# Performance work log

Hardware: AMD Instinct MI355X
Metric: run time of the kernel (lower is better)

Reference implementation:

```python
import jax, jax.numpy as jnp
import numpy as np

BN_EPS = 1e-5


def conv1x1(x, W, b):
    # x: (B, Cin, H, Wd); W: (Cout, Cin); b: (Cout,)
    return jnp.einsum('bchw,oc->bohw', x, W) + b[None, :, None, None]


def maxpool2x2(x):
    B, C, H, Wd = x.shape
    return x.reshape(B, C, H // 2, 2, Wd // 2, 2).max(axis=(3, 5))


def batchnorm_train(x, gamma, beta):
    # training-mode BN over (B, H, W) per channel, NCHW
    mean = x.mean(axis=(0, 2, 3), keepdims=True)
    var = x.var(axis=(0, 2, 3), keepdims=True)
    xn = (x - mean) * jax.lax.rsqrt(var + BN_EPS)
    return xn * gamma[None, :, None, None] + beta[None, :, None, None]


def setup_inputs() -> dict:
    key = jax.random.key(0)
    ks = jax.random.split(key, 11)
    C, Ci = 256, 128
    scale = 1.0 / np.sqrt(C)
    x = jax.random.normal(ks[0], (4, C, 96, 96), dtype=jnp.float32)
    Wg = jax.random.normal(ks[1], (Ci, C), dtype=jnp.float32) * scale
    bg = jax.random.normal(ks[2], (Ci,), dtype=jnp.float32) * 0.01
    Wt = jax.random.normal(ks[3], (Ci, C), dtype=jnp.float32) * scale
    bt = jax.random.normal(ks[4], (Ci,), dtype=jnp.float32) * 0.01
    Wp = jax.random.normal(ks[5], (Ci, C), dtype=jnp.float32) * scale
    bp = jax.random.normal(ks[6], (Ci,), dtype=jnp.float32) * 0.01
    Ww = jax.random.normal(ks[7], (C, Ci), dtype=jnp.float32) * (1.0 / np.sqrt(Ci))
    bw = jax.random.normal(ks[8], (C,), dtype=jnp.float32) * 0.01
    gamma = jax.random.uniform(ks[9], (C,), dtype=jnp.float32)
    beta = jax.random.normal(ks[10], (C,), dtype=jnp.float32) * 0.01
    return {'x': x, 'Wg': Wg, 'bg': bg, 'Wt': Wt, 'bt': bt, 'Wp': Wp,
            'bp': bp, 'Ww': Ww, 'bw': bw, 'gamma': gamma, 'beta': beta}


def reference(x, Wg, bg, Wt, bt, Wp, bp, Ww, bw, gamma, beta):
    B, C, H, Wd = x.shape
    Ci = Wg.shape[0]
    # g, phi: 1x1 conv then 2x2 maxpool (sub_sample_factor=2)
    g_x = maxpool2x2(conv1x1(x, Wg, bg)).reshape(B, Ci, -1)          # (B, Ci, M)
    phi_x = maxpool2x2(conv1x1(x, Wp, bp)).reshape(B, Ci, -1)        # (B, Ci, M)
    theta_x = conv1x1(x, Wt, bt).reshape(B, Ci, -1)                  # (B, Ci, N)
    # embedded-gaussian attention: softmax(theta^T phi) g^T
    f = jnp.einsum('bcn,bcm->bnm', theta_x, phi_x)                   # (B, N, M)
    a = jax.nn.softmax(f, axis=-1)
    y = jnp.einsum('bnm,bcm->bcn', a, g_x).reshape(B, Ci, H, Wd)
    # W: 1x1 conv + BN (training-mode batch stats), then residual
    W_y = batchnorm_train(conv1x1(y, Ww, bw), gamma, beta)
    return W_y + x
```

## Files before the change

kernel.cpp:

```cpp
#include <hip/hip_runtime.h>
#include <hip/hip_bf16.h>

#define BB 4
#define CC 256
#define CI 128
#define NPIX 9216
#define MPIX 2304
#define WIMG 96
#define WPOOL 48
#define LOG2E 1.4426950408889634f

typedef _Float16 f16x2 __attribute__((ext_vector_type(2)));
typedef _Float16 f16x4 __attribute__((ext_vector_type(4)));
typedef _Float16 f16x8 __attribute__((ext_vector_type(8)));
typedef float f32x4 __attribute__((ext_vector_type(4)));

static __device__ __forceinline__ void gload16(const void* g, void* lds) {
  __builtin_amdgcn_global_load_lds(
      (const __attribute__((address_space(1))) unsigned int*)g,
      (__attribute__((address_space(3))) unsigned int*)lds, 16, 0, 0);
}

__global__ __launch_bounds__(256) void k_prep(
    const float* __restrict__ Wt, const float* __restrict__ Wg,
    const float* __restrict__ Wp, const float* __restrict__ Ww,
    _Float16* __restrict__ Wall, _Float16* __restrict__ Wwh)
{
  int i = blockIdx.x * 256 + threadIdx.x;
  if (i < 98304) {
    int o = i >> 8, c = i & 255;
    float v = (o < 128) ? Wt[o * 256 + c]
            : (o < 256) ? Wg[(o - 128) * 256 + c]
                        : Wp[(o - 256) * 256 + c];
    Wall[i] = (_Float16)v;
  } else {
    int j = i - 98304;
    Wwh[j] = (_Float16)Ww[j];
  }
}

__global__ __launch_bounds__(256) void k_xt(
    const float* __restrict__ x, _Float16* __restrict__ xt)
{
  const int nt = blockIdx.x, ct = blockIdx.y, b = blockIdx.z;
  const int n0 = nt * 64, c0 = ct * 64;
  __shared__ float L[64][65];
  const int t = threadIdx.x;
  #pragma unroll
  for (int i = 0; i < 16; ++i) {
    int idx = i * 256 + t, c = idx >> 6, n = idx & 63;
    L[c][n] = x[(size_t)(b * CC + c0 + c) * NPIX + n0 + n];
  }
  __syncthreads();
  #pragma unroll
  for (int i = 0; i < 4; ++i) {
    int idx = i * 256 + t, n = idx >> 4, cg = idx & 15;
    f16x4 v;
    v[0] = (_Float16)L[cg * 4 + 0][n]; v[1] = (_Float16)L[cg * 4 + 1][n];
    v[2] = (_Float16)L[cg * 4 + 2][n]; v[3] = (_Float16)L[cg * 4 + 3][n];
    *(f16x4*)&xt[(size_t)(b * NPIX + n0 + n) * 256 + c0 + cg * 4] = v;
  }
}

__global__ __launch_bounds__(256) void k_convA(
    const _Float16* __restrict__ xt, const _Float16* __restrict__ Wall,
    const float* __restrict__ bt, const float* __restrict__ bg,
    const float* __restrict__ bp,
    _Float16* __restrict__ th_h, _Float16* __restrict__ gphi)
{
  const int pt = blockIdx.x, ot = blockIdx.y, b = blockIdx.z;
  const int p0 = pt * 128, o0 = ot * 128;
  __shared__ char smem[34816];
  char* WsB = smem;
  char* XsB = smem + 8192;
  const int tid = threadIdx.x;
  const int l = tid & 63, w = tid >> 6;
  const int l15 = l & 15, g16 = l >> 4;
  const int wo = (w & 1) * 64, wp = (w >> 1) * 64;

  f32x4 acc[4][4] = {};
  for (int k0 = 0; k0 < 256; k0 += 32) {
    #pragma unroll
    for (int i = 0; i < 2; ++i) {
      int idx = i * 256 + tid, r = idx >> 2, cg = idx & 3;
      int sw = (cg ^ ((r >> 1) & 3)) * 16;
      *(int4*)(WsB + r * 64 + sw) =
          *(const int4*)&Wall[(size_t)(o0 + r) * 256 + k0 + cg * 8];
      *(int4*)(XsB + r * 64 + sw) =
          *(const int4*)&xt[(size_t)(b * NPIX + p0 + r) * 256 + k0 + cg * 8];
    }
    __syncthreads();
    f16x8 af[4], bf[4];
    #pragma unroll
    for (int f = 0; f < 4; ++f) {
      int ro = wo + f * 16 + l15;
      af[f] = *(const f16x8*)(WsB + ro * 64 + ((g16 ^ ((ro >> 1) & 3)) * 16));
      int rp = wp + f * 16 + l15;
      bf[f] = *(const f16x8*)(XsB + rp * 64 + ((g16 ^ ((rp >> 1) & 3)) * 16));
    }
    #pragma unroll
    for (int of = 0; of < 4; ++of)
      #pragma unroll
      for (int pf = 0; pf < 4; ++pf)
        acc[of][pf] = __builtin_amdgcn_mfma_f32_16x16x32_f16(af[of], bf[pf], acc[of][pf], 0, 0, 0);
    __syncthreads();
  }

  if (o0 == 0) {
    _Float16* T = (_Float16*)smem;
    #pragma unroll
    for (int of = 0; of < 4; ++of) {
      const float4 bb = *(const float4*)&bt[wo + of * 16 + g16 * 4];
      float bv[4] = {bb.x, bb.y, bb.z, bb.w};
      #pragma unroll
      for (int pf = 0; pf < 4; ++pf) {
        f16x4 v;
        #pragma unroll
        for (int r = 0; r < 4; ++r)
          v[r] = (_Float16)((acc[of][pf][r] + bv[r]) * LOG2E);
        *(f16x4*)&T[(wp + pf * 16 + l15) * 136 + wo + of * 16 + g16 * 4] = v;
      }
    }
    __syncthreads();
    #pragma unroll
    for (int i = 0; i < 8; ++i) {
      int idx = i * 256 + tid, row = idx >> 4, cg = idx & 15;
      *(int4*)&th_h[(size_t)(b * NPIX + p0 + row) * 128 + cg * 8] =
          *(const int4*)&T[row * 136 + cg * 8];
    }
  } else {
    const float* bsel = (o0 == 128) ? bg : bp;
    const int chbase = o0 - 128;
    #pragma unroll
    for (int of = 0; of < 4; ++of) {
      const float4 bb = *(const float4*)&bsel[wo + of * 16 + g16 * 4];
      float bv[4] = {bb.x, bb.y, bb.z, bb.w};
      #pragma unroll
      for (int pf = 0; pf < 4; ++pf)
        #pragma unroll
        for (int r = 0; r < 4; ++r) {
          int ch = chbase + wo + of * 16 + g16 * 4 + r;
          gphi[(size_t)(b * 256 + ch) * NPIX + p0 + wp + pf * 16 + l15] =
              (_Float16)(acc[of][pf][r] + bv[r]);
        }
    }
  }
}

__global__ __launch_bounds__(256) void k_pool2(
    const _Float16* __restrict__ gphi,
    _Float16* __restrict__ g_h, _Float16* __restrict__ phi_h)
{
  const int mt = blockIdx.x, ct = blockIdx.y, b = blockIdx.z;
  const int m0 = mt * 64, c0 = ct * 32;
  __shared__ _Float16 Lg[32][72], Lp[32][72];
  const int t = threadIdx.x;
  #pragma unroll
  for (int i = 0; i < 8; ++i) {
    int idx = i * 256 + t, c = idx >> 6, m = idx & 63;
    int mm = m0 + m, hp = mm / WPOOL, wp = mm % WPOOL;
    const _Float16* sg = &gphi[(size_t)(b * 256 + c0 + c) * NPIX + hp * 192 + wp * 2];
    f16x2 a0 = *(const f16x2*)sg;
    f16x2 a1 = *(const f16x2*)(sg + WIMG);
    Lg[c][m] = (_Float16)fmaxf(fmaxf((float)a0[0], (float)a0[1]),
                               fmaxf((float)a1[0], (float)a1[1]));
    const _Float16* sp = sg + (size_t)128 * NPIX;
    f16x2 b0 = *(const f16x2*)sp;
    f16x2 b1 = *(const f16x2*)(sp + WIMG);
    Lp[c][m] = (_Float16)fmaxf(fmaxf((float)b0[0], (float)b0[1]),
                               fmaxf((float)b1[0], (float)b1[1]));
  }
  __syncthreads();
  {
    int c = t >> 3, mq = t & 7;
    f16x8 v = *(const f16x8*)&Lg[c][mq * 8];
    *(f16x8*)&g_h[(size_t)(b * CI + c0 + c) * MPIX + m0 + mq * 8] = v;
  }
  #pragma unroll
  for (int i = 0; i < 2; ++i) {
    int idx = i * 256 + t, m = idx >> 3, cg = idx & 7;
    f16x4 v;
    v[0] = Lp[cg * 4 + 0][m]; v[1] = Lp[cg * 4 + 1][m];
    v[2] = Lp[cg * 4 + 2][m]; v[3] = Lp[cg * 4 + 3][m];
    *(f16x4*)&phi_h[(size_t)(b * MPIX + m0 + m) * 128 + c0 + cg * 4] = v;
  }
}

__global__ __launch_bounds__(256, 2) void k_attn(
    const _Float16* __restrict__ th_h,
    const _Float16* __restrict__ phi_h,
    const _Float16* __restrict__ g_h,
    _Float16* __restrict__ y_part,
    float2* __restrict__ ml)
{
  const int qt = blockIdx.x, b = blockIdx.y, split = blockIdx.z;
  const int n0 = qt * 128;
  const int kt0 = split * 18;
  __shared__ char smem[49152];
  char* const GlB = smem + 16384;
  char* const PlB = smem + 32768;

  const int tid = threadIdx.x;
  const int l = tid & 63, wid = tid >> 6;
  const int l15 = l & 15, g16 = l >> 4;
  const int wq0 = wid * 32;

  f16x8 thf[2][4];
  #pragma unroll
  for (int qh = 0; qh < 2; ++qh) {
    const size_t row = (size_t)(b * NPIX + n0 + wq0 + 16 * qh + l15) * 128;
    #pragma unroll
    for (int cs = 0; cs < 4; ++cs)
      thf[qh][cs] = *(const f16x8*)&th_h[row + 32 * cs + 8 * g16];
  }

  auto stage_phi = [&](int kt) {
    const int m1 = kt * 64;
    #pragma unroll
    for (int j = 0; j < 4; ++j) {
      int mbase = wid * 16 + j * 4;
      int m = mbase + (l >> 4);
      int cg = (l & 15) ^ (m & 7);
      gload16(&phi_h[((size_t)(b * MPIX + m1 + m) << 7) + cg * 8],
              smem + mbase * 256);
    }
  };
  auto stage_g = [&](int kt) {
    const int m1 = kt * 64;
    #pragma unroll
    for (int j = 0; j < 4; ++j) {
      int cbase = wid * 32 + j * 8;
      int c = cbase + (l >> 3);
      int cg = (l & 7) ^ (c & 7);
      gload16(&g_h[(size_t)(b * CI + c) * MPIX + m1 + cg * 8],
              GlB + cbase * 128);
    }
  };

  stage_phi(kt0);
  __syncthreads();

  f32x4 yacc[2][8] = {};
  float mrun[2] = {-1e30f, -1e30f};
  float lrun[2] = {0.f, 0.f};

  #pragma unroll 1
  for (int kt = kt0; kt < kt0 + 18; ++kt) {
    stage_g(kt);

    f32x4 sacc[4][2] = {};
    #pragma unroll
    for (int cs = 0; cs < 4; ++cs) {
      const int cb = cs * 64 + g16 * 16;
      #pragma unroll
      for (int mf = 0; mf < 4; ++mf) {
        const int m = 16 * mf + l15;
        f16x8 aph = *(const f16x8*)(smem + m * 256 + (cb ^ ((m & 7) << 4)));
        sacc[mf][0] = __builtin_amdgcn_mfma_f32_16x16x32_f16(aph, thf[0][cs], sacc[mf][0], 0, 0, 0);
        sacc[mf][1] = __builtin_amdgcn_mfma_f32_16x16x32_f16(aph, thf[1][cs], sacc[mf][1], 0, 0, 0);
      }
    }

    float mx[2];
    #pragma unroll
    for (int qh = 0; qh < 2; ++qh) {
      float m0 = -1e30f;
      #pragma unroll
      for (int mf = 0; mf < 4; ++mf)
        #pragma unroll
        for (int r = 0; r < 4; ++r) m0 = fmaxf(m0, sacc[mf][qh][r]);
      m0 = fmaxf(m0, __shfl_xor(m0, 16, 64));
      m0 = fmaxf(m0, __shfl_xor(m0, 32, 64));
      mx[qh] = m0;
    }
    const int nskip = !__all((mx[0] <= mrun[0] + 8.f) & (mx[1] <= mrun[1] + 8.f));
    if (nskip) {
      float scl2[2];
      #pragma unroll
      for (int qh = 0; qh < 2; ++qh) {
        const float mn = fmaxf(mrun[qh], mx[qh]);
        scl2[qh] = exp2f(mrun[qh] - mn);
        lrun[qh] *= scl2[qh];
        mrun[qh] = mn;
      }
      float rs[2][4];
      #pragma unroll
      for (int r = 0; r < 4; ++r) {
        rs[0][r] = __shfl(scl2[0], 4 * g16 + r, 64);
        rs[1][r] = __shfl(scl2[1], 4 * g16 + r, 64);
      }
      #pragma unroll
      for (int qi = 0; qi < 2; ++qi)
        #pragma unroll
        for (int cf = 0; cf < 8; ++cf)
          #pragma unroll
          for (int r = 0; r < 4; ++r)
            yacc[qi][cf][r] *= rs[qi][r];
    }

    f16x4 pr[4][2];
    #pragma unroll
    for (int qh = 0; qh < 2; ++qh) {
      float sum = 0.f;
      #pragma unroll
      for (int mf = 0; mf < 4; ++mf)
        #pragma unroll
        for (int r = 0; r < 4; ++r) {
          float p = exp2f(sacc[mf][qh][r] - mrun[qh]);
          _Float16 ph = (_Float16)p;
          pr[mf][qh][r] = ph;
          sum += (float)ph;
        }
      sum += __shfl_xor(sum, 16, 64);
      sum += __shfl_xor(sum, 32, 64);
      lrun[qh] += sum;
    }

    #pragma unroll
    for (int qh = 0; qh < 2; ++qh) {
      const int qw = l15 + 16 * qh;
      char* prow = PlB + (wid << 12) + qw * 128;
      #pragma unroll
      for (int mf = 0; mf < 4; ++mf)
        *(f16x4*)(prow + ((32 * mf + 8 * g16) ^ ((qw & 7) << 4))) = pr[mf][qh];
    }

    __syncthreads();

    if (kt + 1 < kt0 + 18)
      stage_phi(kt + 1);

    #pragma unroll
    for (int ms = 0; ms < 2; ++ms) {
      const int mb = ms * 64 + g16 * 16;
      const int q0w = l15, q1w = l15 + 16;
      f16x8 pa0 = *(const f16x8*)(PlB + (wid << 12) + q0w * 128 + (mb ^ ((q0w & 7) << 4)));
      f16x8 pa1 = *(const f16x8*)(PlB + (wid << 12) + q1w * 128 + (mb ^ ((q1w & 7) << 4)));
      #pragma unroll
      for (int cf = 0; cf < 8; ++cf) {
        const int c = 16 * cf + l15;
        f16x8 gb = *(const f16x8*)(GlB + c * 128 + (mb ^ ((c & 7) << 4)));
        yacc[0][cf] = __builtin_amdgcn_mfma_f32_16x16x32_f16(pa0, gb, yacc[0][cf], 0, 0, 0);
        yacc[1][cf] = __builtin_amdgcn_mfma_f32_16x16x32_f16(pa1, gb, yacc[1][cf], 0, 0, 0);
      }
    }

    __syncthreads();
  }

  if (g16 == 0) {
    #pragma unroll
    for (int qh = 0; qh < 2; ++qh)
      ml[(size_t)(split * BB + b) * NPIX + n0 + wq0 + 16 * qh + l15] =
          make_float2(mrun[qh], lrun[qh]);
  }
  _Float16* Yl = (_Float16*)smem;
  #pragma unroll
  for (int qi = 0; qi < 2; ++qi)
    #pragma unroll
    for (int cf = 0; cf < 8; ++cf)
      #pragma unroll
      for (int r = 0; r < 4; ++r)
        Yl[(wq0 + 16 * qi + 4 * g16 + r) * 136 + 16 * cf + l15] =
            (_Float16)yacc[qi][cf][r];
  __syncthreads();
  #pragma unroll
  for (int i = 0; i < 8; ++i) {
    int idx = i * 256 + tid, row = idx >> 4, cg = idx & 15;
    *(int4*)&y_part[(size_t)((split * BB + b) * NPIX + n0 + row) * 128 + cg * 8] =
        *(const int4*)&Yl[row * 136 + cg * 8];
  }
}

__global__ __launch_bounds__(256) void k_comb(
    const _Float16* __restrict__ y_part, const float2* __restrict__ ml,
    _Float16* __restrict__ y_h)
{
  int idx = blockIdx.x * 256 + threadIdx.x;
  int cg = idx & 15;
  int n  = (idx >> 4) % NPIX;
  int b  = (idx >> 4) / NPIX;
  float2 a0 = ml[(size_t)b * NPIX + n];
  float2 a1 = ml[(size_t)(BB + b) * NPIX + n];
  float M = fmaxf(a0.x, a1.x);
  float w0 = exp2f(a0.x - M), w1 = exp2f(a1.x - M);
  float inv = 1.0f / (w0 * a0.y + w1 * a1.y);
  w0 *= inv; w1 *= inv;
  f16x8 v0 = *(const f16x8*)&y_part[(size_t)(b * NPIX + n) * 128 + cg * 8];
  f16x8 v1 = *(const f16x8*)&y_part[(size_t)((BB + b) * NPIX + n) * 128 + cg * 8];
  f16x8 o;
  #pragma unroll
  for (int r = 0; r < 8; ++r)
    o[r] = (_Float16)(w0 * (float)v0[r] + w1 * (float)v1[r]);
  *(f16x8*)&y_h[(size_t)(b * NPIX + n) * 128 + cg * 8] = o;
}

__global__ __launch_bounds__(256) void k_wconv(
    const _Float16* __restrict__ y_h, const _Float16* __restrict__ Wwh,
    const float* __restrict__ bw, float* __restrict__ zbuf)
{
  const int nt = blockIdx.x, ot = blockIdx.y, b = blockIdx.z;
  const int n0 = nt * 128, o0 = ot * 128;
  __shared__ char smem[16384];
  char* WsB = smem;
  char* YsB = smem + 8192;
  const int tid = threadIdx.x;
  const int l = tid & 63, w = tid >> 6;
  const int l15 = l & 15, g16 = l >> 4;
  const int wo = (w & 1) * 64, wn = (w >> 1) * 64;

  f32x4 acc[4][4] = {};
  for (int k0 = 0; k0 < 128; k0 += 32) {
    #pragma unroll
    for (int i = 0; i < 2; ++i) {
      int idx = i * 256 + tid, r = idx >> 2, cg = idx & 3;
      int sw = (cg ^ ((r >> 1) & 3)) * 16;
      *(int4*)(WsB + r * 64 + sw) =
          *(const int4*)&Wwh[(size_t)(o0 + r) * 128 + k0 + cg * 8];
      *(int4*)(YsB + r * 64 + sw) =
          *(const int4*)&y_h[(size_t)(b * NPIX + n0 + r) * 128 + k0 + cg * 8];
    }
    __syncthreads();
    f16x8 af[4], bf[4];
    #pragma unroll
    for (int f = 0; f < 4; ++f) {
      int ro = wo + f * 16 + l15;
      af[f] = *(const f16x8*)(WsB + ro * 64 + ((g16 ^ ((ro >> 1) & 3)) * 16));
      int rn = wn + f * 16 + l15;
      bf[f] = *(const f16x8*)(YsB + rn * 64 + ((g16 ^ ((rn >> 1) & 3)) * 16));
    }
    #pragma unroll
    for (int of = 0; of < 4; ++of)
      #pragma unroll
      for (int pf = 0; pf < 4; ++pf)
        acc[of][pf] = __builtin_amdgcn_mfma_f32_16x16x32_f16(af[of], bf[pf], acc[of][pf], 0, 0, 0);
    __syncthreads();
  }
  #pragma unroll
  for (int of = 0; of < 4; ++of) {
    const float4 bb = *(const float4*)&bw[o0 + wo + of * 16 + g16 * 4];
    float bv[4] = {bb.x, bb.y, bb.z, bb.w};
    #pragma unroll
    for (int pf = 0; pf < 4; ++pf)
      #pragma unroll
      for (int r = 0; r < 4; ++r)
        zbuf[(size_t)(b * CC + o0 + wo + of * 16 + g16 * 4 + r) * NPIX +
             n0 + wn + pf * 16 + l15] = acc[of][pf][r] + bv[r];
  }
}

__global__ __launch_bounds__(256) void k_stats(
    const float* __restrict__ zbuf, float* __restrict__ stats)
{
  const int o = blockIdx.x, t = threadIdx.x;
  float s = 0.f, s2 = 0.f;
  for (int b = 0; b < BB; ++b) {
    const float* z = &zbuf[(size_t)(b * CC + o) * NPIX];
    for (int i = t; i < NPIX / 4; i += 256) {
      float4 v = *(const float4*)&z[i * 4];
      s  += v.x + v.y + v.z + v.w;
      s2 += v.x * v.x + v.y * v.y + v.z * v.z + v.w * v.w;
    }
  }
  #pragma unroll
  for (int off = 1; off < 64; off <<= 1) {
    s  += __shfl_xor(s,  off, 64);
    s2 += __shfl_xor(s2, off, 64);
  }
  __shared__ float ls[4], ls2[4];
  if ((t & 63) == 0) { ls[t >> 6] = s; ls2[t >> 6] = s2; }
  __syncthreads();
  if (t == 0) {
    float S  = ls[0] + ls[1] + ls[2] + ls[3];
    float S2 = ls2[0] + ls2[1] + ls2[2] + ls2[3];
    const float invn = 1.0f / (float)(BB * NPIX);
    float mean = S * invn;
    float var  = S2 * invn - mean * mean;
    stats[o] = mean;
    stats[CC + o] = rsqrtf(var + 1e-5f);
  }
}

__global__ __launch_bounds__(256) void k_out(
    const float* __restrict__ zbuf, const float* __restrict__ x,
    const float* __restrict__ gamma, const float* __restrict__ beta,
    const float* __restrict__ stats, float* __restrict__ out)
{
  int idx = blockIdx.x * 256 + threadIdx.x;
  const int total4 = BB * CC * NPIX / 4;
  if (idx >= total4) return;
  size_t e = (size_t)idx * 4;
  int p = (int)(e % NPIX);
  int o = (int)((e / NPIX) % CC);
  int b = (int)(e / ((size_t)CC * NPIX));
  float a  = stats[CC + o] * gamma[o];
  float c0 = beta[o] - stats[o] * a;
  float4 z  = *(const float4*)&zbuf[(size_t)(b * CC + o) * NPIX + p];
  float4 xv = *(const float4*)&x[e];
  float4 rv;
  rv.x = z.x * a + c0 + xv.x;
  rv.y = z.y * a + c0 + xv.y;
  rv.z = z.z * a + c0 + xv.z;
  rv.w = z.w * a + c0 + xv.w;
  *(float4*)&out[e] = rv;
}

extern "C" void kernel_launch(void* const* d_in, const int* in_sizes, int n_in,
                              void* d_out, int out_size, void* d_ws, size_t ws_size,
                              hipStream_t stream)
{
  const float* x     = (const float*)d_in[0];
  const float* Wg    = (const float*)d_in[1];
  const float* bg    = (const float*)d_in[2];
  const float* Wt    = (const float*)d_in[3];
  const float* bt    = (const float*)d_in[4];
  const float* Wp    = (const float*)d_in[5];
  const float* bp    = (const float*)d_in[6];
  const float* Ww    = (const float*)d_in[7];
  const float* bw    = (const float*)d_in[8];
  const float* gamma = (const float*)d_in[9];
  const float* beta  = (const float*)d_in[10];
  float* out = (float*)d_out;

  char* wsb = (char*)d_ws;
  float*    zbuf   = (float*)wsb;
  _Float16* xt     = (_Float16*)wsb;
  _Float16* y_part = (_Float16*)wsb;
  char* p2 = wsb + 37748736;
  _Float16* gphi  = (_Float16*)p2;
  _Float16* y_h   = (_Float16*)p2;
  char* p3 = p2 + 18874368;
  _Float16* th_h  = (_Float16*)p3;
  _Float16* g_h   = (_Float16*)(p3 + 9437184);
  _Float16* phi_h = (_Float16*)(p3 + 11796480);
  _Float16* Wall  = (_Float16*)(p3 + 14155776);
  _Float16* Wwh   = (_Float16*)(p3 + 14352384);
  float*    stats = (float*)(p3 + 14417920);
  float2*   ml    = (float2*)(p3 + 14420992);

  k_prep<<<512, 256, 0, stream>>>(Wt, Wg, Wp, Ww, Wall, Wwh);

  dim3 gxt(NPIX / 64, CC / 64, BB);
  k_xt<<<gxt, 256, 0, stream>>>(x, xt);

  dim3 g1(NPIX / 128, 3, BB);
  k_convA<<<g1, 256, 0, stream>>>(xt, Wall, bt, bg, bp, th_h, gphi);

  dim3 g2(MPIX / 64, 4, BB);
  k_pool2<<<g2, 256, 0, stream>>>(gphi, g_h, phi_h);

  dim3 g3(NPIX / 128, BB, 2);
  k_attn<<<g3, 256, 0, stream>>>(th_h, phi_h, g_h, y_part, ml);

  k_comb<<<(BB * NPIX * 16) / 256, 256, 0, stream>>>(y_part, ml, y_h);

  dim3 g4(NPIX / 128, CC / 128, BB);
  k_wconv<<<g4, 256, 0, stream>>>(y_h, Wwh, bw, zbuf);

  k_stats<<<CC, 256, 0, stream>>>(zbuf, stats);

  k_out<<<(BB * CC * NPIX / 4 + 255) / 256, 256, 0, stream>>>(zbuf, x, gamma, beta, stats, out);
}
```

Measured before the change: 184.4 us.

## Fuse BN statistics into W-conv epilogue, store fp16 intermediate, simplify softmax rescale

The W-conv epilogue now accumulates per-channel sum and sum-of-squares with shuffles and atomics, and writes z as fp16 instead of fp32. This removes the separate stats kernel's full pass over z and halves the z traffic in both the write and the output kernel. A tiny finalize kernel and a memset are added. The attention loop also drops the lazy-rescale skip branch and always rescales, merging the max, exp and sum passes. Storing z in fp16 and using float atomics add rounding error and make the statistics order-dependent.

```diff
diff --git a/kernel.cpp b/kernel.cpp
--- a/kernel.cpp
+++ b/kernel.cpp
@@ -261,28 +261,47 @@
       }
     }
 
-    float mx[2];
+    float scl2[2];
+    f16x4 pr[4][2];
     #pragma unroll
     for (int qh = 0; qh < 2; ++qh) {
-      float m0 = -1e30f;
+      float mx = -1e30f;
       #pragma unroll
       for (int mf = 0; mf < 4; ++mf)
         #pragma unroll
-        for (int r = 0; r < 4; ++r) m0 = fmaxf(m0, sacc[mf][qh][r]);
-      m0 = fmaxf(m0, __shfl_xor(m0, 16, 64));
-      m0 = fmaxf(m0, __shfl_xor(m0, 32, 64));
-      mx[qh] = m0;
-    }
-    const int nskip = !__all((mx[0] <= mrun[0] + 8.f) & (mx[1] <= mrun[1] + 8.f));
-    if (nskip) {
-      float scl2[2];
-      #pragma unroll
-      for (int qh = 0; qh < 2; ++qh) {
-        const float mn = fmaxf(mrun[qh], mx[qh]);
-        scl2[qh] = exp2f(mrun[qh] - mn);
-        lrun[qh] *= scl2[qh];
-        mrun[qh] = mn;
-      }
+        for (int r = 0; r < 4; ++r) mx = fmaxf(mx, sacc[mf][qh][r]);
+      mx = fmaxf(mx, __shfl_xor(mx, 16, 64));
+      mx = fmaxf(mx, __shfl_xor(mx, 32, 64));
+      const float mo = mrun[qh];
+      const float mn = fmaxf(mo, mx);
+      float sum = 0.f;
+      #pragma unroll
+      for (int mf = 0; mf < 4; ++mf)
+        #pragma unroll
+        for (int r = 0; r < 4; ++r) {
+          float p = exp2f(sacc[mf][qh][r] - mn);
+          _Float16 ph = (_Float16)p;
+          pr[mf][qh][r] = ph;
+          sum += (float)ph;
+        }
+      sum += __shfl_xor(sum, 16, 64);
+      sum += __shfl_xor(sum, 32, 64);
+      const float sc = exp2f(mo - mn);
+      scl2[qh] = sc;
+      lrun[qh] = lrun[qh] * sc + sum;
+      mrun[qh] = mn;
+    }
+
+    #pragma unroll
+    for (int qh = 0; qh < 2; ++qh) {
+      const int qw = l15 + 16 * qh;
+      char* prow = PlB + (wid << 12) + qw * 128;
+      #pragma unroll
+      for (int mf = 0; mf < 4; ++mf)
+        *(f16x4*)(prow + ((32 * mf + 8 * g16) ^ ((qw & 7) << 4))) = pr[mf][qh];
+    }
+
+    {
       float rs[2][4];
       #pragma unroll
       for (int r = 0; r < 4; ++r) {
@@ -296,33 +315,6 @@
           #pragma unroll
           for (int r = 0; r < 4; ++r)
             yacc[qi][cf][r] *= rs[qi][r];
-    }
-
-    f16x4 pr[4][2];
-    #pragma unroll
-    for (int qh = 0; qh < 2; ++qh) {
-      float sum = 0.f;
-      #pragma unroll
-      for (int mf = 0; mf < 4; ++mf)
-        #pragma unroll
-        for (int r = 0; r < 4; ++r) {
-          float p = exp2f(sacc[mf][qh][r] - mrun[qh]);
-          _Float16 ph = (_Float16)p;
-          pr[mf][qh][r] = ph;
-          sum += (float)ph;
-        }
-      sum += __shfl_xor(sum, 16, 64);
-      sum += __shfl_xor(sum, 32, 64);
-      lrun[qh] += sum;
-    }
-
-    #pragma unroll
-    for (int qh = 0; qh < 2; ++qh) {
-      const int qw = l15 + 16 * qh;
-      char* prow = PlB + (wid << 12) + qw * 128;
-      #pragma unroll
-      for (int mf = 0; mf < 4; ++mf)
-        *(f16x4*)(prow + ((32 * mf + 8 * g16) ^ ((qw & 7) << 4))) = pr[mf][qh];
     }
 
     __syncthreads();
@@ -397,7 +389,8 @@
 
 __global__ __launch_bounds__(256) void k_wconv(
     const _Float16* __restrict__ y_h, const _Float16* __restrict__ Wwh,
-    const float* __restrict__ bw, float* __restrict__ zbuf)
+    const float* __restrict__ bw, _Float16* __restrict__ z_h,
+    float* __restrict__ statsum)
 {
   const int nt = blockIdx.x, ot = blockIdx.y, b = blockIdx.z;
   const int n0 = nt * 128, o0 = ot * 128;
@@ -441,68 +434,67 @@
     const float4 bb = *(const float4*)&bw[o0 + wo + of * 16 + g16 * 4];
     float bv[4] = {bb.x, bb.y, bb.z, bb.w};
     #pragma unroll
-    for (int pf = 0; pf < 4; ++pf)
-      #pragma unroll
-      for (int r = 0; r < 4; ++r)
-        zbuf[(size_t)(b * CC + o0 + wo + of * 16 + g16 * 4 + r) * NPIX +
-             n0 + wn + pf * 16 + l15] = acc[of][pf][r] + bv[r];
-  }
-}
-
-__global__ __launch_bounds__(256) void k_stats(
-    const float* __restrict__ zbuf, float* __restrict__ stats)
-{
-  const int o = blockIdx.x, t = threadIdx.x;
-  float s = 0.f, s2 = 0.f;
-  for (int b = 0; b < BB; ++b) {
-    const float* z = &zbuf[(size_t)(b * CC + o) * NPIX];
-    for (int i = t; i < NPIX / 4; i += 256) {
-      float4 v = *(const float4*)&z[i * 4];
-      s  += v.x + v.y + v.z + v.w;
-      s2 += v.x * v.x + v.y * v.y + v.z * v.z + v.w * v.w;
-    }
-  }
-  #pragma unroll
-  for (int off = 1; off < 64; off <<= 1) {
-    s  += __shfl_xor(s,  off, 64);
-    s2 += __shfl_xor(s2, off, 64);
-  }
-  __shared__ float ls[4], ls2[4];
-  if ((t & 63) == 0) { ls[t >> 6] = s; ls2[t >> 6] = s2; }
-  __syncthreads();
-  if (t == 0) {
-    float S  = ls[0] + ls[1] + ls[2] + ls[3];
-    float S2 = ls2[0] + ls2[1] + ls2[2] + ls2[3];
-    const float invn = 1.0f / (float)(BB * NPIX);
-    float mean = S * invn;
-    float var  = S2 * invn - mean * mean;
-    stats[o] = mean;
-    stats[CC + o] = rsqrtf(var + 1e-5f);
-  }
+    for (int r = 0; r < 4; ++r) {
+      const int o = o0 + wo + of * 16 + g16 * 4 + r;
+      float s = 0.f, s2 = 0.f;
+      #pragma unroll
+      for (int pf = 0; pf < 4; ++pf) {
+        float zv = acc[of][pf][r] + bv[r];
+        s += zv; s2 += zv * zv;
+        z_h[(size_t)(b * CC + o) * NPIX + n0 + wn + pf * 16 + l15] = (_Float16)zv;
+      }
+      #pragma unroll
+      for (int off = 1; off < 16; off <<= 1) {
+        s  += __shfl_xor(s,  off, 64);
+        s2 += __shfl_xor(s2, off, 64);
+      }
+      if (l15 == 0) {
+        atomicAdd(&statsum[o], s);
+        atomicAdd(&statsum[CC + o], s2);
+      }
+    }
+  }
+}
+
+__global__ __launch_bounds__(256) void k_finstat(
+    const float* __restrict__ statsum, float* __restrict__ stats)
+{
+  int o = threadIdx.x;
+  const float invn = 1.0f / (float)(BB * NPIX);
+  float mean = statsum[o] * invn;
+  float var  = statsum[CC + o] * invn - mean * mean;
+  stats[o] = mean;
+  stats[CC + o] = rsqrtf(var + 1e-5f);
 }
 
 __global__ __launch_bounds__(256) void k_out(
-    const float* __restrict__ zbuf, const float* __restrict__ x,
+    const _Float16* __restrict__ z_h, const float* __restrict__ x,
     const float* __restrict__ gamma, const float* __restrict__ beta,
     const float* __restrict__ stats, float* __restrict__ out)
 {
   int idx = blockIdx.x * 256 + threadIdx.x;
-  const int total4 = BB * CC * NPIX / 4;
-  if (idx >= total4) return;
-  size_t e = (size_t)idx * 4;
+  const int total8 = BB * CC * NPIX / 8;
+  if (idx >= total8) return;
+  size_t e = (size_t)idx * 8;
   int p = (int)(e % NPIX);
   int o = (int)((e / NPIX) % CC);
   int b = (int)(e / ((size_t)CC * NPIX));
   float a  = stats[CC + o] * gamma[o];
   float c0 = beta[o] - stats[o] * a;
-  float4 z  = *(const float4*)&zbuf[(size_t)(b * CC + o) * NPIX + p];
-  float4 xv = *(const float4*)&x[e];
-  float4 rv;
-  rv.x = z.x * a + c0 + xv.x;
-  rv.y = z.y * a + c0 + xv.y;
-  rv.z = z.z * a + c0 + xv.z;
-  rv.w = z.w * a + c0 + xv.w;
-  *(float4*)&out[e] = rv;
+  f16x8 z = *(const f16x8*)&z_h[(size_t)(b * CC + o) * NPIX + p];
+  float4 x0 = *(const float4*)&x[e];
+  float4 x1 = *(const float4*)&x[e + 4];
+  float4 r0, r1;
+  r0.x = (float)z[0] * a + c0 + x0.x;
+  r0.y = (float)z[1] * a + c0 + x0.y;
+  r0.z = (float)z[2] * a + c0 + x0.z;
+  r0.w = (float)z[3] * a + c0 + x0.w;
+  r1.x = (float)z[4] * a + c0 + x1.x;
+  r1.y = (float)z[5] * a + c0 + x1.y;
+  r1.z = (float)z[6] * a + c0 + x1.z;
+  r1.w = (float)z[7] * a + c0 + x1.w;
+  *(float4*)&out[e] = r0;
+  *(float4*)&out[e + 4] = r1;
 }
 
 extern "C" void kernel_launch(void* const* d_in, const int* in_sizes, int n_in,
@@ -523,22 +515,25 @@
   float* out = (float*)d_out;
 
   char* wsb = (char*)d_ws;
-  float*    zbuf   = (float*)wsb;
   _Float16* xt     = (_Float16*)wsb;
   _Float16* y_part = (_Float16*)wsb;
+  _Float16* z_h    = (_Float16*)wsb;
   char* p2 = wsb + 37748736;
   _Float16* gphi  = (_Float16*)p2;
   _Float16* y_h   = (_Float16*)p2;
   char* p3 = p2 + 18874368;
-  _Float16* th_h  = (_Float16*)p3;
-  _Float16* g_h   = (_Float16*)(p3 + 9437184);
-  _Float16* phi_h = (_Float16*)(p3 + 11796480);
-  _Float16* Wall  = (_Float16*)(p3 + 14155776);
-  _Float16* Wwh   = (_Float16*)(p3 + 14352384);
-  float*    stats = (float*)(p3 + 14417920);
-  float2*   ml    = (float2*)(p3 + 14420992);
+  _Float16* th_h    = (_Float16*)p3;
+  _Float16* g_h     = (_Float16*)(p3 + 9437184);
+  _Float16* phi_h   = (_Float16*)(p3 + 11796480);
+  _Float16* Wall    = (_Float16*)(p3 + 14155776);
+  _Float16* Wwh     = (_Float16*)(p3 + 14352384);
+  float*    statsum = (float*)(p3 + 14417920);
+  float2*   ml      = (float2*)(p3 + 14420992);
+  float*    stats   = (float*)(p3 + 14420992 + 589824);
 
   k_prep<<<512, 256, 0, stream>>>(Wt, Wg, Wp, Ww, Wall, Wwh);
+
+  hipMemsetAsync(statsum, 0, 2048, stream);
 
   dim3 gxt(NPIX / 64, CC / 64, BB);
   k_xt<<<gxt, 256, 0, stream>>>(x, xt);
@@ -555,9 +550,9 @@
   k_comb<<<(BB * NPIX * 16) / 256, 256, 0, stream>>>(y_part, ml, y_h);
 
   dim3 g4(NPIX / 128, CC / 128, BB);
-  k_wconv<<<g4, 256, 0, stream>>>(y_h, Wwh, bw, zbuf);
-
-  k_stats<<<CC, 256, 0, stream>>>(zbuf, stats);
-
-  k_out<<<(BB * CC * NPIX / 4 + 255) / 256, 256, 0, stream>>>(zbuf, x, gamma, beta, stats, out);
-}
+  k_wconv<<<g4, 256, 0, stream>>>(y_h, Wwh, bw, z_h, statsum);
+
+  k_finstat<<<1, 256, 0, stream>>>(statsum, stats);
+
+  k_out<<<(BB * CC * NPIX / 8 + 255) / 256, 256, 0, stream>>>(z_h, x, gamma, beta, stats, out);
+}
```

Result: slower. 243.9 us (+32.2%).
